# Performance work log

Hardware: AMD Instinct MI355X
Metric: run time of the kernel (lower is better)

Reference implementation:

```python
import jax, jax.numpy as jnp
import numpy as np

VOCAB = 50257
EMBED = 256
NFREQ = 64
NRULES = 100
B, S = 4, 1024


def setup_inputs() -> dict:
    key = jax.random.key(0)
    ks = jax.random.split(key, 7)
    return {
        "token_ids": jax.random.randint(ks[0], (B, S), 0, VOCAB),
        "a_n": jax.random.normal(ks[1], (VOCAB, NFREQ), dtype=jnp.float32),
        "b_n": jax.random.normal(ks[2], (VOCAB, NFREQ), dtype=jnp.float32),
        "rule_transform": jax.random.normal(ks[3], (NRULES, EMBED, EMBED), dtype=jnp.float32),
        "token_rules": jax.random.randint(ks[4], (VOCAB,), 0, NRULES),
        "proj_w": jax.random.normal(ks[5], (EMBED, NFREQ), dtype=jnp.float32) * (1.0 / np.sqrt(NFREQ)),
        "proj_b": jax.random.normal(ks[6], (EMBED,), dtype=jnp.float32) * 0.01,
    }


def reference(token_ids, a_n, b_n, rule_transform, token_rules, proj_w, proj_b):
    vocab_size, nfreq = a_n.shape
    # fourier_freqs = linspace(1, F, F) -> [1..F]
    freqs = jnp.arange(1, nfreq + 1, dtype=jnp.float32)  # [F]
    x = token_ids.astype(jnp.float32)[..., None] / vocab_size  # [B,S,1]
    ang = (2.0 * jnp.pi) * freqs * x  # [B,S,F]
    # gather per-token fourier coefficients, fuse cos/sin combine
    fourier = a_n[token_ids] * jnp.cos(ang) + b_n[token_ids] * jnp.sin(ang)  # [B,S,F]
    base = jnp.einsum('bsf,df->bsd', fourier, proj_w) + proj_b  # [B,S,D]
    rule_idx = token_rules[token_ids]  # [B,S]
    rules = rule_transform[rule_idx]  # [B,S,D,D] gathered per token
    return jnp.einsum('bsd,bsde->bse', base, rules)  # [B,S,D]
```

## Files before the change

### kernel.cpp

```cpp
#include <hip/hip_runtime.h>
#include <math.h>

#define VOCAB   50257
#define EMBED   256
#define NFREQ   64
#define NRULES  100
#define NTOK    4096
#define CAP     256
#define CHUNK   16
#define NCHUNK  8

typedef __attribute__((ext_vector_type(8))) short short8;
typedef __attribute__((ext_vector_type(4))) float floatx4;

#define BASEBF_BYTES ((size_t)NTOK * EMBED * 2)
#define LIST_BYTES   ((size_t)NRULES * CAP * 4)
#define CNT_OFF      (BASEBF_BYTES)
#define LIST_OFF     (CNT_OFF + 512)
#define WT_OFF       (LIST_OFF + LIST_BYTES)
#define TFRAG_OFF    (WT_OFF + (size_t)NFREQ * EMBED * 4)

__device__ __forceinline__ ushort f2bf(float f) {
    unsigned u = __float_as_uint(f);
    unsigned r = (u + 0x7FFFu + ((u >> 16) & 1u)) >> 16;
    return (ushort)r;
}

__global__ __launch_bounds__(256) void prep_convert_bucket_kernel(
    const float* __restrict__ T,
    const float* __restrict__ proj_w,
    const int*   __restrict__ token_ids,
    const int*   __restrict__ token_rules,
    ushort*      __restrict__ Tfrag,
    float*       __restrict__ wT,
    int*         __restrict__ counts,
    int*         __restrict__ list)
{
    __shared__ float s[32 * 260];
    const int tid = threadIdx.x;

    if (blockIdx.x < NRULES) {
        const int r  = blockIdx.x;
        const int kb = blockIdx.y;

        const float4* __restrict__ src =
            (const float4*)(T + (size_t)r * 65536 + (size_t)kb * 32 * 256);
        #pragma unroll
        for (int i = 0; i < 8; ++i) {
            const int v   = i * 256 + tid;
            const int row = v >> 6, c4 = v & 63;
            ((float4*)s)[row * 65 + c4] = src[v];
        }
        __syncthreads();

        const int et  = tid >> 4;
        const int l16 = tid & 15;
        uint4* __restrict__ dst = (uint4*)Tfrag + (size_t)r * 16384;

        #pragma unroll
        for (int lg = 0; lg < 4; ++lg) {
            ushort h[8];
            #pragma unroll
            for (int j = 0; j < 8; ++j)
                h[j] = f2bf(s[(lg * 8 + j) * 260 + et * 16 + l16]);
            uint4 o;
            o.x = (unsigned)h[0] | ((unsigned)h[1] << 16);
            o.y = (unsigned)h[2] | ((unsigned)h[3] << 16);
            o.z = (unsigned)h[4] | ((unsigned)h[5] << 16);
            o.w = (unsigned)h[6] | ((unsigned)h[7] << 16);
            dst[(et * 8 + kb) * 64 + lg * 16 + l16] = o;
        }
        return;
    }

    if (blockIdx.y < 4) {
        const int b = blockIdx.y;
        const float4* __restrict__ W4 =
            (const float4*)(proj_w + (size_t)b * 64 * NFREQ);
        #pragma unroll
        for (int i = 0; i < 4; ++i) {
            const int v = i * 256 + tid;
            const float4 w = W4[v];
            const int dl = v >> 4, f0 = (v & 15) * 4;
            s[dl * 65 + f0 + 0] = w.x;
            s[dl * 65 + f0 + 1] = w.y;
            s[dl * 65 + f0 + 2] = w.z;
            s[dl * 65 + f0 + 3] = w.w;
        }
        __syncthreads();
        #pragma unroll
        for (int j = 0; j < 16; ++j) {
            const int o = j * 256 + tid;
            const int f = o >> 6, c = o & 63;
            wT[f * EMBED + b * 64 + c] = s[c * 65 + f];
        }
        return;
    }

    if (blockIdx.y == 4) {
        int* s_cnt = (int*)s;
        if (tid < NRULES) s_cnt[tid] = 0;
        __syncthreads();
        for (int i = tid; i < NTOK; i += 256) {
            const int tok  = token_ids[i];
            const int rule = token_rules[tok];
            const int pos  = atomicAdd(&s_cnt[rule], 1);
            if (pos < CAP) list[rule * CAP + pos] = i;
        }
        __syncthreads();
        if (tid < NRULES) counts[tid] = s_cnt[tid];
    }
}

__global__ __launch_bounds__(256) void fused_base_kernel(
    const int*   __restrict__ token_ids,
    const float* __restrict__ a_n,
    const float* __restrict__ b_n,
    const float* __restrict__ wT,
    const float* __restrict__ proj_b,
    ushort*      __restrict__ base_bf)
{
    __shared__ float s_four[4][NFREQ];

    const int tid = threadIdx.x;
    const int tl  = tid >> 6;
    const int f   = tid & 63;
    const int tok_idx = blockIdx.x * 4 + tl;
    const int tok     = token_ids[tok_idx];

    const float x   = (float)tok * (1.0f / (float)VOCAB);
    const float rev = (float)(f + 1) * x;
    const float rf  = rev - floorf(rev);
    const float sv  = __builtin_amdgcn_sinf(rf);
    const float cv  = __builtin_amdgcn_cosf(rf);
    s_four[tl][f] = a_n[(size_t)tok * NFREQ + f] * cv
                  + b_n[(size_t)tok * NFREQ + f] * sv;
    __syncthreads();

    const int   d    = tid;
    const float bias = proj_b[d];
    float a0 = bias, a1 = bias, a2 = bias, a3 = bias;

    #pragma unroll 4
    for (int q = 0; q < 16; ++q) {
        const float w0 = wT[(4 * q + 0) * EMBED + d];
        const float w1 = wT[(4 * q + 1) * EMBED + d];
        const float w2 = wT[(4 * q + 2) * EMBED + d];
        const float w3 = wT[(4 * q + 3) * EMBED + d];
        const float4 f0 = ((const float4*)s_four[0])[q];
        const float4 f1 = ((const float4*)s_four[1])[q];
        const float4 f2 = ((const float4*)s_four[2])[q];
        const float4 f3 = ((const float4*)s_four[3])[q];
        a0 += w0 * f0.x + w1 * f0.y + w2 * f0.z + w3 * f0.w;
        a1 += w0 * f1.x + w1 * f1.y + w2 * f1.z + w3 * f1.w;
        a2 += w0 * f2.x + w1 * f2.y + w2 * f2.z + w3 * f2.w;
        a3 += w0 * f3.x + w1 * f3.y + w2 * f3.z + w3 * f3.w;
    }
    base_bf[(size_t)(blockIdx.x * 4 + 0) * EMBED + d] = f2bf(a0);
    base_bf[(size_t)(blockIdx.x * 4 + 1) * EMBED + d] = f2bf(a1);
    base_bf[(size_t)(blockIdx.x * 4 + 2) * EMBED + d] = f2bf(a2);
    base_bf[(size_t)(blockIdx.x * 4 + 3) * EMBED + d] = f2bf(a3);
}

__global__ __launch_bounds__(256) void apply_kernel(
    const ushort* __restrict__ base_bf,
    const ushort* __restrict__ Tfrag,
    const int*    __restrict__ counts,
    const int*    __restrict__ list,
    float*        __restrict__ out)
{
    __shared__ __align__(16) ushort s_a[16 * 264];

    const int rule = blockIdx.x;
    int cnt = counts[rule];
    if (cnt > CAP) cnt = CAP;
    const int t0 = blockIdx.y * CHUNK;
    if (t0 >= cnt) return;

    const int tid  = threadIdx.x;
    const int w    = tid >> 6;
    const int lane = tid & 63;

    const int* __restrict__ lst = list + rule * CAP;
    int idx[CHUNK];
    #pragma unroll
    for (int t = 0; t < CHUNK; ++t) {
        int tt = t0 + t;
        if (tt > cnt - 1) tt = cnt - 1;
        idx[t] = __builtin_amdgcn_readfirstlane(lst[tt]);
    }

    #pragma unroll
    for (int i = 0; i < 2; ++i) {
        const int v = i * 256 + tid;
        const int t = v >> 5, c = v & 31;
        ((uint4*)s_a)[t * 33 + c] =
            ((const uint4*)(base_bf + (size_t)idx[t] * EMBED))[c];
    }
    __syncthreads();

    const short8* __restrict__ Bf =
        (const short8*)Tfrag + (size_t)rule * 16384;

    floatx4 acc[4];
    #pragma unroll
    for (int q = 0; q < 4; ++q) acc[q] = (floatx4){0.f, 0.f, 0.f, 0.f};

    const int arow = (lane & 15) * 33 + (lane >> 4);

    short8 bcur[4], bnxt[4];
    #pragma unroll
    for (int q = 0; q < 4; ++q)
        bcur[q] = Bf[((w * 4 + q) * 8 + 0) * 64 + lane];

    for (int kb = 0; kb < 8; ++kb) {
        if (kb < 7) {
            #pragma unroll
            for (int q = 0; q < 4; ++q)
                bnxt[q] = Bf[((w * 4 + q) * 8 + kb + 1) * 64 + lane];
        }
        const short8 av = ((const short8*)s_a)[arow + kb * 4];
        #pragma unroll
        for (int q = 0; q < 4; ++q)
            acc[q] = __builtin_amdgcn_mfma_f32_16x16x32_bf16(
                av, bcur[q], acc[q], 0, 0, 0);
        #pragma unroll
        for (int q = 0; q < 4; ++q) bcur[q] = bnxt[q];
    }

    const int m4 = (lane >> 4) * 4;
    const int n  = lane & 15;
    #pragma unroll
    for (int q = 0; q < 4; ++q) {
        const int e = (w * 4 + q) * 16 + n;
        #pragma unroll
        for (int r = 0; r < 4; ++r) {
            const int m = m4 + r;
            if (t0 + m < cnt)
                out[(size_t)idx[m] * EMBED + e] = acc[q][r];
        }
    }
}

extern "C" void kernel_launch(void* const* d_in, const int* in_sizes, int n_in,
                              void* d_out, int out_size, void* d_ws, size_t ws_size,
                              hipStream_t stream) {
    const int*   token_ids      = (const int*)  d_in[0];
    const float* a_n            = (const float*)d_in[1];
    const float* b_n            = (const float*)d_in[2];
    const float* rule_transform = (const float*)d_in[3];
    const int*   token_rules    = (const int*)  d_in[4];
    const float* proj_w         = (const float*)d_in[5];
    const float* proj_b         = (const float*)d_in[6];
    float*       out            = (float*)d_out;

    ushort* base_bf = (ushort*)d_ws;
    int*    counts  = (int*)   ((char*)d_ws + CNT_OFF);
    int*    list    = (int*)   ((char*)d_ws + LIST_OFF);
    float*  wT      = (float*) ((char*)d_ws + WT_OFF);
    ushort* Tfrag   = (ushort*)((char*)d_ws + TFRAG_OFF);

    prep_convert_bucket_kernel<<<dim3(NRULES + 1, 8), 256, 0, stream>>>(
        rule_transform, proj_w, token_ids, token_rules,
        Tfrag, wT, counts, list);
    fused_base_kernel<<<NTOK / 4, 256, 0, stream>>>(
        token_ids, a_n, b_n, wT, proj_b, base_bf);
    apply_kernel<<<dim3(NRULES, NCHUNK), 256, 0, stream>>>(
        base_bf, Tfrag, counts, list, out);
}
```

Before: 121.7 us.

## Fold projection into per-rule transforms and fuse base computation into apply

Precomputes per-rule folded weights W_r = proj_w^T · T_r (64x256) and bias proj_b · T_r with MFMA, using a split-bf16 (hi+lo) representation of T. The apply kernel then computes the Fourier features per token directly and multiplies by the folded 64-wide weights, so the separate base kernel and the 256-wide K reduction go away. The intent is to cut one launch and most of the per-token FLOPs and intermediate traffic, at the cost of a heavier prep kernel (100 rules × 64×256×256 GEMM) and extra bf16 rounding of the folded weights.

```diff
diff --git a/kernel.cpp b/kernel.cpp
--- a/kernel.cpp
+++ b/kernel.cpp
@@ -9,16 +9,16 @@
 #define CAP     256
 #define CHUNK   16
 #define NCHUNK  8
+#define ESPLIT  2
+#define ECOLS   (EMBED / ESPLIT)
 
 typedef __attribute__((ext_vector_type(8))) short short8;
 typedef __attribute__((ext_vector_type(4))) float floatx4;
 
-#define BASEBF_BYTES ((size_t)NTOK * EMBED * 2)
-#define LIST_BYTES   ((size_t)NRULES * CAP * 4)
-#define CNT_OFF      (BASEBF_BYTES)
-#define LIST_OFF     (CNT_OFF + 512)
-#define WT_OFF       (LIST_OFF + LIST_BYTES)
-#define TFRAG_OFF    (WT_OFF + (size_t)NFREQ * EMBED * 4)
+#define CNT_OFF   0
+#define LIST_OFF  512
+#define BR_OFF    (LIST_OFF + (size_t)NRULES * CAP * 4)
+#define WFRAG_OFF (BR_OFF + (size_t)NRULES * EMBED * 4)
 
 __device__ __forceinline__ ushort f2bf(float f) {
     unsigned u = __float_as_uint(f);
@@ -26,79 +26,25 @@
     return (ushort)r;
 }
 
-__global__ __launch_bounds__(256) void prep_convert_bucket_kernel(
+__global__ __launch_bounds__(256) void fold_kernel(
     const float* __restrict__ T,
     const float* __restrict__ proj_w,
+    const float* __restrict__ proj_b,
     const int*   __restrict__ token_ids,
     const int*   __restrict__ token_rules,
-    ushort*      __restrict__ Tfrag,
-    float*       __restrict__ wT,
+    ushort*      __restrict__ Wfrag,
+    float*       __restrict__ br,
     int*         __restrict__ counts,
     int*         __restrict__ list)
 {
-    __shared__ float s[32 * 260];
+    __shared__ __align__(16) ushort s_a[80 * 264];
+    __shared__ __align__(16) float  s_t[32 * 132];
+
     const int tid = threadIdx.x;
 
-    if (blockIdx.x < NRULES) {
-        const int r  = blockIdx.x;
-        const int kb = blockIdx.y;
-
-        const float4* __restrict__ src =
-            (const float4*)(T + (size_t)r * 65536 + (size_t)kb * 32 * 256);
-        #pragma unroll
-        for (int i = 0; i < 8; ++i) {
-            const int v   = i * 256 + tid;
-            const int row = v >> 6, c4 = v & 63;
-            ((float4*)s)[row * 65 + c4] = src[v];
-        }
-        __syncthreads();
-
-        const int et  = tid >> 4;
-        const int l16 = tid & 15;
-        uint4* __restrict__ dst = (uint4*)Tfrag + (size_t)r * 16384;
-
-        #pragma unroll
-        for (int lg = 0; lg < 4; ++lg) {
-            ushort h[8];
-            #pragma unroll
-            for (int j = 0; j < 8; ++j)
-                h[j] = f2bf(s[(lg * 8 + j) * 260 + et * 16 + l16]);
-            uint4 o;
-            o.x = (unsigned)h[0] | ((unsigned)h[1] << 16);
-            o.y = (unsigned)h[2] | ((unsigned)h[3] << 16);
-            o.z = (unsigned)h[4] | ((unsigned)h[5] << 16);
-            o.w = (unsigned)h[6] | ((unsigned)h[7] << 16);
-            dst[(et * 8 + kb) * 64 + lg * 16 + l16] = o;
-        }
-        return;
-    }
-
-    if (blockIdx.y < 4) {
-        const int b = blockIdx.y;
-        const float4* __restrict__ W4 =
-            (const float4*)(proj_w + (size_t)b * 64 * NFREQ);
-        #pragma unroll
-        for (int i = 0; i < 4; ++i) {
-            const int v = i * 256 + tid;
-            const float4 w = W4[v];
-            const int dl = v >> 4, f0 = (v & 15) * 4;
-            s[dl * 65 + f0 + 0] = w.x;
-            s[dl * 65 + f0 + 1] = w.y;
-            s[dl * 65 + f0 + 2] = w.z;
-            s[dl * 65 + f0 + 3] = w.w;
-        }
-        __syncthreads();
-        #pragma unroll
-        for (int j = 0; j < 16; ++j) {
-            const int o = j * 256 + tid;
-            const int f = o >> 6, c = o & 63;
-            wT[f * EMBED + b * 64 + c] = s[c * 65 + f];
-        }
-        return;
-    }
-
-    if (blockIdx.y == 4) {
-        int* s_cnt = (int*)s;
+    if (blockIdx.x == NRULES) {
+        if (blockIdx.y != 0) return;
+        int* s_cnt = (int*)s_a;
         if (tid < NRULES) s_cnt[tid] = 0;
         __syncthreads();
         for (int i = tid; i < NTOK; i += 256) {
@@ -109,67 +55,129 @@
         }
         __syncthreads();
         if (tid < NRULES) counts[tid] = s_cnt[tid];
-    }
-}
-
-__global__ __launch_bounds__(256) void fused_base_kernel(
-    const int*   __restrict__ token_ids,
-    const float* __restrict__ a_n,
-    const float* __restrict__ b_n,
-    const float* __restrict__ wT,
-    const float* __restrict__ proj_b,
-    ushort*      __restrict__ base_bf)
-{
-    __shared__ float s_four[4][NFREQ];
-
-    const int tid = threadIdx.x;
-    const int tl  = tid >> 6;
-    const int f   = tid & 63;
-    const int tok_idx = blockIdx.x * 4 + tl;
-    const int tok     = token_ids[tok_idx];
-
-    const float x   = (float)tok * (1.0f / (float)VOCAB);
-    const float rev = (float)(f + 1) * x;
-    const float rf  = rev - floorf(rev);
-    const float sv  = __builtin_amdgcn_sinf(rf);
-    const float cv  = __builtin_amdgcn_cosf(rf);
-    s_four[tl][f] = a_n[(size_t)tok * NFREQ + f] * cv
-                  + b_n[(size_t)tok * NFREQ + f] * sv;
+        return;
+    }
+
+    const int r  = blockIdx.x;
+    const int eh = blockIdx.y;
+    const float* __restrict__ Tr = T + (size_t)r * 65536 + (size_t)eh * ECOLS;
+
+    float4 pf[4];
+    #pragma unroll
+    for (int i = 0; i < 4; ++i) {
+        const int v = i * 256 + tid;
+        pf[i] = ((const float4*)(Tr + (size_t)(v >> 5) * 256))[v & 31];
+    }
+
+    {
+        const float4* __restrict__ pw4 = (const float4*)proj_w;
+        #pragma unroll
+        for (int i = 0; i < 16; ++i) {
+            const int v = i * 256 + tid;
+            const int d = v >> 4, f0 = (v & 15) * 4;
+            const float4 wv = pw4[v];
+            s_a[(f0 + 0) * 264 + d] = f2bf(wv.x);
+            s_a[(f0 + 1) * 264 + d] = f2bf(wv.y);
+            s_a[(f0 + 2) * 264 + d] = f2bf(wv.z);
+            s_a[(f0 + 3) * 264 + d] = f2bf(wv.w);
+        }
+        s_a[64 * 264 + tid] = f2bf(proj_b[tid]);
+        for (int i = tid; i < 15 * 264; i += 256) s_a[65 * 264 + i] = 0;
+    }
+
+    const int w    = tid >> 6;
+    const int lane = tid & 63;
+    const int l16  = lane & 15, lg = lane >> 4;
+
+    floatx4 acc[2][5];
+    #pragma unroll
+    for (int q = 0; q < 2; ++q)
+        #pragma unroll
+        for (int mt = 0; mt < 5; ++mt) acc[q][mt] = (floatx4){0.f, 0.f, 0.f, 0.f};
+
+    for (int kb = 0; kb < 8; ++kb) {
+        __syncthreads();
+        #pragma unroll
+        for (int i = 0; i < 4; ++i) {
+            const int v = i * 256 + tid;
+            ((float4*)(s_t + (v >> 5) * 132))[v & 31] = pf[i];
+        }
+        if (kb < 7) {
+            #pragma unroll
+            for (int i = 0; i < 4; ++i) {
+                const int v = i * 256 + tid;
+                pf[i] = ((const float4*)(Tr + (size_t)((kb + 1) * 32 + (v >> 5)) * 256))[v & 31];
+            }
+        }
+        __syncthreads();
+
+        short8 bh[2], bl[2];
+        #pragma unroll
+        for (int q = 0; q < 2; ++q) {
+            #pragma unroll
+            for (int j = 0; j < 8; ++j) {
+                const float  tv = s_t[(lg * 8 + j) * 132 + (w * 2 + q) * 16 + l16];
+                const ushort h  = f2bf(tv);
+                const float  hf = __uint_as_float((unsigned)h << 16);
+                bh[q][j] = (short)h;
+                bl[q][j] = (short)f2bf(tv - hf);
+            }
+        }
+        #pragma unroll
+        for (int mt = 0; mt < 5; ++mt) {
+            const short8 ah = *(const short8*)(s_a + (mt * 16 + l16) * 264 + kb * 32 + lg * 8);
+            #pragma unroll
+            for (int q = 0; q < 2; ++q) {
+                acc[q][mt] = __builtin_amdgcn_mfma_f32_16x16x32_bf16(ah, bh[q], acc[q][mt], 0, 0, 0);
+                acc[q][mt] = __builtin_amdgcn_mfma_f32_16x16x32_bf16(ah, bl[q], acc[q][mt], 0, 0, 0);
+            }
+        }
+    }
     __syncthreads();
 
-    const int   d    = tid;
-    const float bias = proj_b[d];
-    float a0 = bias, a1 = bias, a2 = bias, a3 = bias;
-
-    #pragma unroll 4
-    for (int q = 0; q < 16; ++q) {
-        const float w0 = wT[(4 * q + 0) * EMBED + d];
-        const float w1 = wT[(4 * q + 1) * EMBED + d];
-        const float w2 = wT[(4 * q + 2) * EMBED + d];
-        const float w3 = wT[(4 * q + 3) * EMBED + d];
-        const float4 f0 = ((const float4*)s_four[0])[q];
-        const float4 f1 = ((const float4*)s_four[1])[q];
-        const float4 f2 = ((const float4*)s_four[2])[q];
-        const float4 f3 = ((const float4*)s_four[3])[q];
-        a0 += w0 * f0.x + w1 * f0.y + w2 * f0.z + w3 * f0.w;
-        a1 += w0 * f1.x + w1 * f1.y + w2 * f1.z + w3 * f1.w;
-        a2 += w0 * f2.x + w1 * f2.y + w2 * f2.z + w3 * f2.w;
-        a3 += w0 * f3.x + w1 * f3.y + w2 * f3.z + w3 * f3.w;
-    }
-    base_bf[(size_t)(blockIdx.x * 4 + 0) * EMBED + d] = f2bf(a0);
-    base_bf[(size_t)(blockIdx.x * 4 + 1) * EMBED + d] = f2bf(a1);
-    base_bf[(size_t)(blockIdx.x * 4 + 2) * EMBED + d] = f2bf(a2);
-    base_bf[(size_t)(blockIdx.x * 4 + 3) * EMBED + d] = f2bf(a3);
-}
-
-__global__ __launch_bounds__(256) void apply_kernel(
-    const ushort* __restrict__ base_bf,
-    const ushort* __restrict__ Tfrag,
+    ushort* wtmp = (ushort*)s_t;
+    #pragma unroll
+    for (int q = 0; q < 2; ++q) {
+        const int e_l = (w * 2 + q) * 16 + l16;
+        #pragma unroll
+        for (int mt = 0; mt < 4; ++mt)
+            #pragma unroll
+            for (int rr = 0; rr < 4; ++rr)
+                wtmp[(mt * 16 + lg * 4 + rr) * 130 + e_l] = f2bf(acc[q][mt][rr]);
+        if (lg == 0)
+            br[(size_t)r * EMBED + eh * ECOLS + e_l] = acc[q][4][0];
+    }
+    __syncthreads();
+
+    uint4* __restrict__ dst = (uint4*)Wfrag + (size_t)r * 2048;
+    #pragma unroll
+    for (int ii = 0; ii < 4; ++ii) {
+        const int v   = ii * 256 + tid;
+        const int etl = v >> 7, kbb = (v >> 6) & 1, ln = v & 63;
+        ushort h[8];
+        #pragma unroll
+        for (int j = 0; j < 8; ++j)
+            h[j] = wtmp[(kbb * 32 + (ln >> 4) * 8 + j) * 130 + etl * 16 + (ln & 15)];
+        uint4 o;
+        o.x = (unsigned)h[0] | ((unsigned)h[1] << 16);
+        o.y = (unsigned)h[2] | ((unsigned)h[3] << 16);
+        o.z = (unsigned)h[4] | ((unsigned)h[5] << 16);
+        o.w = (unsigned)h[6] | ((unsigned)h[7] << 16);
+        dst[((eh * 8 + etl) * 2 + kbb) * 64 + ln] = o;
+    }
+}
+
+__global__ __launch_bounds__(256) void apply_fold_kernel(
+    const int*    __restrict__ token_ids,
+    const float*  __restrict__ a_n,
+    const float*  __restrict__ b_n,
+    const ushort* __restrict__ Wfrag,
+    const float*  __restrict__ br,
     const int*    __restrict__ counts,
     const int*    __restrict__ list,
     float*        __restrict__ out)
 {
-    __shared__ __align__(16) ushort s_a[16 * 264];
+    __shared__ __align__(16) ushort s_f[16 * 72];
 
     const int rule = blockIdx.x;
     int cnt = counts[rule];
@@ -180,8 +188,25 @@
     const int tid  = threadIdx.x;
     const int w    = tid >> 6;
     const int lane = tid & 63;
+    const int l16  = lane & 15;
 
     const int* __restrict__ lst = list + rule * CAP;
+
+    const short8* __restrict__ Bf = (const short8*)Wfrag + (size_t)rule * 2048;
+    short8 bw[4][2];
+    #pragma unroll
+    for (int q = 0; q < 4; ++q)
+        #pragma unroll
+        for (int kb = 0; kb < 2; ++kb)
+            bw[q][kb] = Bf[((w * 4 + q) * 2 + kb) * 64 + lane];
+
+    floatx4 acc[4];
+    #pragma unroll
+    for (int q = 0; q < 4; ++q) {
+        const float brv = br[(size_t)rule * EMBED + (w * 4 + q) * 16 + l16];
+        acc[q] = (floatx4){brv, brv, brv, brv};
+    }
+
     int idx[CHUNK];
     #pragma unroll
     for (int t = 0; t < CHUNK; ++t) {
@@ -190,49 +215,44 @@
         idx[t] = __builtin_amdgcn_readfirstlane(lst[tt]);
     }
 
-    #pragma unroll
-    for (int i = 0; i < 2; ++i) {
-        const int v = i * 256 + tid;
-        const int t = v >> 5, c = v & 31;
-        ((uint4*)s_a)[t * 33 + c] =
-            ((const uint4*)(base_bf + (size_t)idx[t] * EMBED))[c];
+    {
+        const int tloc = tid >> 4, fg = tid & 15;
+        int tt = t0 + tloc; if (tt > cnt - 1) tt = cnt - 1;
+        const int tok  = token_ids[lst[tt]];
+        const float x  = (float)tok * (1.0f / (float)VOCAB);
+        const float4 av = ((const float4*)(a_n + (size_t)tok * NFREQ))[fg];
+        const float4 bv = ((const float4*)(b_n + (size_t)tok * NFREQ))[fg];
+        const float aa[4] = {av.x, av.y, av.z, av.w};
+        const float bb[4] = {bv.x, bv.y, bv.z, bv.w};
+        ushort h[4];
+        #pragma unroll
+        for (int i = 0; i < 4; ++i) {
+            const float rev = (float)(fg * 4 + i + 1) * x;
+            const float rf  = rev - floorf(rev);
+            const float sv  = __builtin_amdgcn_sinf(rf);
+            const float cv  = __builtin_amdgcn_cosf(rf);
+            h[i] = f2bf(aa[i] * cv + bb[i] * sv);
+        }
+        uint2 o;
+        o.x = (unsigned)h[0] | ((unsigned)h[1] << 16);
+        o.y = (unsigned)h[2] | ((unsigned)h[3] << 16);
+        *(uint2*)(s_f + tloc * 72 + fg * 4) = o;
     }
     __syncthreads();
 
-    const short8* __restrict__ Bf =
-        (const short8*)Tfrag + (size_t)rule * 16384;
-
-    floatx4 acc[4];
-    #pragma unroll
-    for (int q = 0; q < 4; ++q) acc[q] = (floatx4){0.f, 0.f, 0.f, 0.f};
-
-    const int arow = (lane & 15) * 33 + (lane >> 4);
-
-    short8 bcur[4], bnxt[4];
-    #pragma unroll
-    for (int q = 0; q < 4; ++q)
-        bcur[q] = Bf[((w * 4 + q) * 8 + 0) * 64 + lane];
-
-    for (int kb = 0; kb < 8; ++kb) {
-        if (kb < 7) {
-            #pragma unroll
-            for (int q = 0; q < 4; ++q)
-                bnxt[q] = Bf[((w * 4 + q) * 8 + kb + 1) * 64 + lane];
-        }
-        const short8 av = ((const short8*)s_a)[arow + kb * 4];
+    const int arow = l16 * 72 + (lane >> 4) * 8;
+    #pragma unroll
+    for (int kb = 0; kb < 2; ++kb) {
+        const short8 av8 = *(const short8*)(s_f + arow + kb * 32);
         #pragma unroll
         for (int q = 0; q < 4; ++q)
-            acc[q] = __builtin_amdgcn_mfma_f32_16x16x32_bf16(
-                av, bcur[q], acc[q], 0, 0, 0);
-        #pragma unroll
-        for (int q = 0; q < 4; ++q) bcur[q] = bnxt[q];
+            acc[q] = __builtin_amdgcn_mfma_f32_16x16x32_bf16(av8, bw[q][kb], acc[q], 0, 0, 0);
     }
 
     const int m4 = (lane >> 4) * 4;
-    const int n  = lane & 15;
     #pragma unroll
     for (int q = 0; q < 4; ++q) {
-        const int e = (w * 4 + q) * 16 + n;
+        const int e = (w * 4 + q) * 16 + l16;
         #pragma unroll
         for (int r = 0; r < 4; ++r) {
             const int m = m4 + r;
@@ -254,17 +274,14 @@
     const float* proj_b         = (const float*)d_in[6];
     float*       out            = (float*)d_out;
 
-    ushort* base_bf = (ushort*)d_ws;
-    int*    counts  = (int*)   ((char*)d_ws + CNT_OFF);
-    int*    list    = (int*)   ((char*)d_ws + LIST_OFF);
-    float*  wT      = (float*) ((char*)d_ws + WT_OFF);
-    ushort* Tfrag   = (ushort*)((char*)d_ws + TFRAG_OFF);
-
-    prep_convert_bucket_kernel<<<dim3(NRULES + 1, 8), 256, 0, stream>>>(
-        rule_transform, proj_w, token_ids, token_rules,
-        Tfrag, wT, counts, list);
-    fused_base_kernel<<<NTOK / 4, 256, 0, stream>>>(
-        token_ids, a_n, b_n, wT, proj_b, base_bf);
-    apply_kernel<<<dim3(NRULES, NCHUNK), 256, 0, stream>>>(
-        base_bf, Tfrag, counts, list, out);
-}
+    int*    counts = (int*)   ((char*)d_ws + CNT_OFF);
+    int*    list   = (int*)   ((char*)d_ws + LIST_OFF);
+    float*  brp    = (float*) ((char*)d_ws + BR_OFF);
+    ushort* Wfrag  = (ushort*)((char*)d_ws + WFRAG_OFF);
+
+    fold_kernel<<<dim3(NRULES + 1, ESPLIT), 256, 0, stream>>>(
+        rule_transform, proj_w, proj_b, token_ids, token_rules,
+        Wfrag, brp, counts, list);
+    apply_fold_kernel<<<dim3(NRULES, NCHUNK), 256, 0, stream>>>(
+        token_ids, a_n, b_n, Wfrag, brp, counts, list, out);
+}
```

Result: no change. 120.6 us (-0.9%).
